# Performance work log

Measured on AMD Instinct MI355X. Metric: run time of the kernel, lower is better.

The kernel has to match this reference:

```python
import jax, jax.numpy as jnp
import numpy as np

ITERATIONS = 3  # init_kwargs: adjacency power order

def setup_inputs() -> dict:
    key = jax.random.key(0)
    ks = jax.random.split(key, 8)
    n_nodes = 100000
    in_ch, out_ch = 512, 128
    nnz_feat = 1600000
    n_edges = 1600000
    feat_rows = jax.random.randint(ks[0], (nnz_feat,), 0, n_nodes, dtype=jnp.int32)
    feat_cols = jax.random.randint(ks[1], (nnz_feat,), 0, in_ch, dtype=jnp.int32)
    feat_values = jax.random.uniform(ks[2], (nnz_feat,), dtype=jnp.float32)
    adj_rows = jax.random.randint(ks[3], (n_edges,), 0, n_nodes, dtype=jnp.int32)
    adj_cols = jax.random.randint(ks[4], (n_edges,), 0, n_nodes, dtype=jnp.int32)
    # normalized adjacency values (positive, roughly 1/degree scale)
    adj_values = jax.random.uniform(ks[5], (n_edges,), dtype=jnp.float32) / 16.0
    # xavier-uniform-like init
    bound_w = float(np.sqrt(6.0 / (in_ch + out_ch)))
    weight = jax.random.uniform(ks[6], (in_ch, out_ch), minval=-bound_w, maxval=bound_w, dtype=jnp.float32)
    bound_b = float(np.sqrt(6.0 / (1 + out_ch)))
    bias = jax.random.uniform(ks[7], (1, out_ch), minval=-bound_b, maxval=bound_b, dtype=jnp.float32)
    return {"feat_rows": feat_rows, "feat_cols": feat_cols, "feat_values": feat_values,
            "adj_rows": adj_rows, "adj_cols": adj_cols, "adj_values": adj_values,
            "weight": weight, "bias": bias, "n_nodes": n_nodes}

def reference(feat_rows, feat_cols, feat_values, adj_rows, adj_cols, adj_values, weight, bias, n_nodes):
    # SpMM: (sparse features [n_nodes, in_ch]) @ weight [in_ch, out_ch]
    # base[r] = sum over nnz with row r of val * weight[col]
    contrib = feat_values[:, None] * weight[feat_cols]           # [nnz, out_ch]
    base = jax.ops.segment_sum(contrib, feat_rows, num_segments=n_nodes)  # [n_nodes, out_ch]
    # bias + dropout (eval mode: identity) + relu
    base = jax.nn.relu(base + bias)
    # iterative sparse propagation: base = A_norm @ base, (iterations - 1) times
    for _ in range(ITERATIONS - 1):
        msgs = adj_values[:, None] * base[adj_cols]              # [n_edges, out_ch]
        base = jax.ops.segment_sum(msgs, adj_rows, num_segments=n_nodes)
    return base
```

## Files before the change

kernel.cpp:

```cpp
#include <hip/hip_runtime.h>
#include <hip/hip_fp16.h>


#define CH 128
#define BR 128
#define SCAN_BLK 1024
#define BIN_WGS 256
#define BIN_THR 512


__global__ void hist2_kernel(const int* __restrict__ rows_f, int nf, int chunk_f,
                             const int* __restrict__ rows_a, int na, int chunk_a,
                             int* __restrict__ wgc, int nbuck) {
    extern __shared__ int hcnt[];
    const int m  = blockIdx.x >> 8;
    const int wg = blockIdx.x & (BIN_WGS - 1);
    const int* rows = m ? rows_a : rows_f;
    const int nE    = m ? na : nf;
    const int chunk = m ? chunk_a : chunk_f;
    const int tid = threadIdx.x;
    const long long T = blockDim.x;
    long long start = (long long)wg * chunk;
    long long end = start + chunk;
    if (end > nE) end = nE;
    for (int b = tid; b < nbuck; b += blockDim.x) hcnt[b] = 0;
    __syncthreads();
    if (start < end) {
        long long i = start + tid;
        for (; i + 3 * T < end; i += 4 * T) {
            int r0 = rows[i], r1 = rows[i + T], r2 = rows[i + 2 * T], r3 = rows[i + 3 * T];
            atomicAdd(&hcnt[r0 >> 7], 1);
            atomicAdd(&hcnt[r1 >> 7], 1);
            atomicAdd(&hcnt[r2 >> 7], 1);
            atomicAdd(&hcnt[r3 >> 7], 1);
        }
        for (; i < end; i += T) atomicAdd(&hcnt[rows[i] >> 7], 1);
    }
    __syncthreads();
    int* out = wgc + ((long long)m * BIN_WGS + wg) * nbuck;
    for (int b = tid; b < nbuck; b += blockDim.x) out[b] = hcnt[b];
}

__global__ void wgscan2_kernel(int* __restrict__ wgc, int* __restrict__ bcounts,
                               int nbuck, int nwg) {
    int wpb = blockDim.x >> 6;
    int idx = blockIdx.x * wpb + (threadIdx.x >> 6);
    int lane = threadIdx.x & 63;
    if (idx >= 2 * nbuck) return;
    int m = (idx >= nbuck) ? 1 : 0;
    int b = idx - m * nbuck;
    int* base = wgc + (long long)m * nwg * nbuck + b;
    int carry = 0;
    for (int w0 = 0; w0 < nwg; w0 += 64) {
        int wg = w0 + lane;
        int v = (wg < nwg) ? base[(long long)wg * nbuck] : 0;
        int x = v;
        #pragma unroll
        for (int off = 1; off < 64; off <<= 1) {
            int y = __shfl_up(x, off);
            if (lane >= off) x += y;
        }
        if (wg < nwg) base[(long long)wg * nbuck] = carry + x - v;
        carry += __shfl(x, 63);
    }
    if (lane == 0) bcounts[idx] = carry;
}

__global__ void bucket_scan2_kernel(const int* __restrict__ bcounts,
                                    int* __restrict__ bbase, int nbuck) {
    __shared__ int lds[SCAN_BLK];
    int m = blockIdx.x;
    int tid = threadIdx.x;
    int x = (tid < nbuck) ? bcounts[m * nbuck + tid] : 0;
    lds[tid] = x;
    __syncthreads();
    for (int off = 1; off < SCAN_BLK; off <<= 1) {
        int y = (tid >= off) ? lds[tid - off] : 0;
        __syncthreads();
        lds[tid] += y;
        __syncthreads();
    }
    int* bb = bbase + m * (nbuck + 1);
    if (tid < nbuck) bb[tid] = lds[tid] - x;
    if (tid == nbuck - 1) bb[nbuck] = lds[tid];
}

__global__ void bin2_kernel(const int* __restrict__ rows_f, const int* __restrict__ cols_f,
                            const float* __restrict__ vals_f, int nf, int chunk_f,
                            const int* __restrict__ rows_a, const int* __restrict__ cols_a,
                            const float* __restrict__ vals_a, int na, int chunk_a,
                            const int* __restrict__ bbase, const int* __restrict__ wgc,
                            int2* __restrict__ cvt_f, int2* __restrict__ cvt_a, int nbuck) {
    extern __shared__ int lds[];
    int* hcnt  = lds;
    int* hbase = lds + nbuck;
    const int m  = blockIdx.x >> 8;
    const int wg = blockIdx.x & (BIN_WGS - 1);
    const int* rows = m ? rows_a : rows_f;
    const int* cols = m ? cols_a : cols_f;
    const float* vals = m ? vals_a : vals_f;
    const int nE    = m ? na : nf;
    const int chunk = m ? chunk_a : chunk_f;
    int2* cv_tmp = m ? cvt_a : cvt_f;
    const int* bb = bbase + m * (nbuck + 1);
    const int* wc = wgc + ((long long)m * BIN_WGS + wg) * nbuck;
    const int tid = threadIdx.x;
    const long long T = blockDim.x;
    long long start = (long long)wg * chunk;
    long long end = start + chunk;
    if (end > nE) end = nE;
    for (int b = tid; b < nbuck; b += blockDim.x) {
        hbase[b] = bb[b] + wc[b];
        hcnt[b] = 0;
    }
    __syncthreads();
    if (start >= end) return;
    long long i = start + tid;
    for (; i + 3 * T < end; i += 4 * T) {
        int r0 = rows[i], r1 = rows[i + T], r2 = rows[i + 2 * T], r3 = rows[i + 3 * T];
        int c0 = cols[i], c1 = cols[i + T], c2 = cols[i + 2 * T], c3 = cols[i + 3 * T];
        float v0 = vals[i], v1 = vals[i + T], v2 = vals[i + 2 * T], v3 = vals[i + 3 * T];
        int b0 = r0 >> 7, b1 = r1 >> 7, b2 = r2 >> 7, b3 = r3 >> 7;
        int p0 = hbase[b0] + atomicAdd(&hcnt[b0], 1);
        int p1 = hbase[b1] + atomicAdd(&hcnt[b1], 1);
        int p2 = hbase[b2] + atomicAdd(&hcnt[b2], 1);
        int p3 = hbase[b3] + atomicAdd(&hcnt[b3], 1);
        cv_tmp[p0] = make_int2(c0 | ((r0 & (BR - 1)) << 24), __float_as_int(v0));
        cv_tmp[p1] = make_int2(c1 | ((r1 & (BR - 1)) << 24), __float_as_int(v1));
        cv_tmp[p2] = make_int2(c2 | ((r2 & (BR - 1)) << 24), __float_as_int(v2));
        cv_tmp[p3] = make_int2(c3 | ((r3 & (BR - 1)) << 24), __float_as_int(v3));
    }
    for (; i < end; i += T) {
        int r = rows[i];
        int b = r >> 7;
        int p = hbase[b] + atomicAdd(&hcnt[b], 1);
        cv_tmp[p] = make_int2(cols[i] | ((r & (BR - 1)) << 24), __float_as_int(vals[i]));
    }
}

__global__ void reorder2_kernel(const int* __restrict__ bucket_base,
                                const int2* __restrict__ cv_tmp, int2* __restrict__ cv,
                                int* __restrict__ row_ptr, int n) {
    __shared__ int cnt[BR];
    __shared__ int tmp[BR];
    int b = blockIdx.x;
    int rbase = b * BR;
    int tid = threadIdx.x;
    int s = bucket_base[b], e = bucket_base[b + 1];
    if (tid < BR) cnt[tid] = 0;
    __syncthreads();
    for (int i = s + tid; i < e; i += blockDim.x)
        atomicAdd(&cnt[((unsigned)cv_tmp[i].x) >> 24], 1);
    __syncthreads();
    if (tid < BR) tmp[tid] = cnt[tid];
    __syncthreads();
    for (int off = 1; off < BR; off <<= 1) {
        int y = 0;
        if (tid < BR && tid >= off) y = tmp[tid - off];
        __syncthreads();
        if (tid < BR) tmp[tid] += y;
        __syncthreads();
    }
    if (tid < BR) {
        int excl = s + tmp[tid] - cnt[tid];
        if (rbase + tid < n) row_ptr[rbase + tid] = excl;
        cnt[tid] = excl;
    }
    if (tid == 0 && b == gridDim.x - 1) row_ptr[n] = e;
    __syncthreads();
    for (int i = s + tid; i < e; i += blockDim.x) {
        int2 ent = cv_tmp[i];
        int rl = ((unsigned)ent.x) >> 24;
        int p = atomicAdd(&cnt[rl], 1);
        cv[p] = make_int2(ent.x & 0x00FFFFFF, ent.y);
    }
}


__global__ void wconv_kernel(const float* __restrict__ W, __half2* __restrict__ Wh, int n2) {
    int i = blockIdx.x * blockDim.x + threadIdx.x;
    if (i < n2) Wh[i] = __float22half2_rn(reinterpret_cast<const float2*>(W)[i]);
}


#define GATHER_BODY(TBL)                                                            \
    for (int base = s; base < e; base += 64) {                                      \
        int idx = base + lane;                                                      \
        mysc[lane] = (idx < e) ? cv[idx] : 0;                                       \
        int m = e - base; if (m > 64) m = 64;                                       \
        int nb = (m + 15) >> 4;                                                     \
        for (int t = 0; t < nb; t++) {                                              \
            int k0 = t << 4;                                                        \
            long long ck0 = mysc[k0 + g];                                           \
            long long ck1 = mysc[k0 + 4 + g];                                       \
            long long ck2 = mysc[k0 + 8 + g];                                       \
            long long ck3 = mysc[k0 + 12 + g];                                      \
            float4 sv0 = *reinterpret_cast<const float4*>(TBL + (long long)(int)ck0 * 64 + cl * 4); \
            float4 sv1 = *reinterpret_cast<const float4*>(TBL + (long long)(int)ck1 * 64 + cl * 4); \
            float4 sv2 = *reinterpret_cast<const float4*>(TBL + (long long)(int)ck2 * 64 + cl * 4); \
            float4 sv3 = *reinterpret_cast<const float4*>(TBL + (long long)(int)ck3 * 64 + cl * 4); \
            float v0 = __int_as_float((int)(ck0 >> 32));                            \
            float v1 = __int_as_float((int)(ck1 >> 32));                            \
            float v2 = __int_as_float((int)(ck2 >> 32));                            \
            float v3 = __int_as_float((int)(ck3 >> 32));                            \
            ACC8(v0, sv0); ACC8(v1, sv1); ACC8(v2, sv2); ACC8(v3, sv3);             \
        }                                                                           \
    }

#define ACC8(V, SV) {                                                               \
    float2 f0 = __half22float2(*reinterpret_cast<const __half2*>(&(SV).x));         \
    float2 f1 = __half22float2(*reinterpret_cast<const __half2*>(&(SV).y));         \
    float2 f2 = __half22float2(*reinterpret_cast<const __half2*>(&(SV).z));         \
    float2 f3 = __half22float2(*reinterpret_cast<const __half2*>(&(SV).w));         \
    acc0 += (V) * f0.x; acc1 += (V) * f0.y;                                         \
    acc2 += (V) * f1.x; acc3 += (V) * f1.y;                                         \
    acc4 += (V) * f2.x; acc5 += (V) * f2.y;                                         \
    acc6 += (V) * f3.x; acc7 += (V) * f3.y; }

#define XREDUCE()                                                                   \
    acc0 += __shfl_xor(acc0, 16); acc1 += __shfl_xor(acc1, 16);                     \
    acc2 += __shfl_xor(acc2, 16); acc3 += __shfl_xor(acc3, 16);                     \
    acc4 += __shfl_xor(acc4, 16); acc5 += __shfl_xor(acc5, 16);                     \
    acc6 += __shfl_xor(acc6, 16); acc7 += __shfl_xor(acc7, 16);                     \
    acc0 += __shfl_xor(acc0, 32); acc1 += __shfl_xor(acc1, 32);                     \
    acc2 += __shfl_xor(acc2, 32); acc3 += __shfl_xor(acc3, 32);                     \
    acc4 += __shfl_xor(acc4, 32); acc5 += __shfl_xor(acc5, 32);                     \
    acc6 += __shfl_xor(acc6, 32); acc7 += __shfl_xor(acc7, 32);

__global__ void spmm_g4_kernel(const int* __restrict__ row_ptr,
                               const long long* __restrict__ cv,
                               const __half2* __restrict__ Wh,
                               const float* __restrict__ bias,
                               __half2* __restrict__ outh, int n) {
    __shared__ long long sc[4 * 64];
    int gtid = blockIdx.x * blockDim.x + threadIdx.x;
    int wid = gtid >> 6;
    int lane = gtid & 63;
    if (wid >= n) return;
    int g = lane >> 4;
    int cl = lane & 15;
    long long* mysc = sc + (threadIdx.x >> 6) * 64;
    int s = row_ptr[wid], e = row_ptr[wid + 1];
    float acc0 = 0.f, acc1 = 0.f, acc2 = 0.f, acc3 = 0.f;
    float acc4 = 0.f, acc5 = 0.f, acc6 = 0.f, acc7 = 0.f;
    GATHER_BODY(Wh)
    XREDUCE()
    if (g == 0) {
        const float4* bp = reinterpret_cast<const float4*>(bias);
        float4 b0 = bp[cl * 2], b1 = bp[cl * 2 + 1];
        acc0 = fmaxf(acc0 + b0.x, 0.f); acc1 = fmaxf(acc1 + b0.y, 0.f);
        acc2 = fmaxf(acc2 + b0.z, 0.f); acc3 = fmaxf(acc3 + b0.w, 0.f);
        acc4 = fmaxf(acc4 + b1.x, 0.f); acc5 = fmaxf(acc5 + b1.y, 0.f);
        acc6 = fmaxf(acc6 + b1.z, 0.f); acc7 = fmaxf(acc7 + b1.w, 0.f);
        __half2 h0 = __floats2half2_rn(acc0, acc1);
        __half2 h1 = __floats2half2_rn(acc2, acc3);
        __half2 h2 = __floats2half2_rn(acc4, acc5);
        __half2 h3 = __floats2half2_rn(acc6, acc7);
        float4 ov;
        *reinterpret_cast<__half2*>(&ov.x) = h0;
        *reinterpret_cast<__half2*>(&ov.y) = h1;
        *reinterpret_cast<__half2*>(&ov.z) = h2;
        *reinterpret_cast<__half2*>(&ov.w) = h3;
        *reinterpret_cast<float4*>(outh + (long long)wid * 64 + cl * 4) = ov;
    }
}

__global__ void prop_g4_h2h_kernel(const int* __restrict__ row_ptr,
                                   const long long* __restrict__ cv,
                                   const __half2* __restrict__ src, __half2* __restrict__ dst,
                                   int n) {
    __shared__ long long sc[4 * 64];
    int gtid = blockIdx.x * blockDim.x + threadIdx.x;
    int wid = gtid >> 6;
    int lane = gtid & 63;
    if (wid >= n) return;
    int g = lane >> 4;
    int cl = lane & 15;
    long long* mysc = sc + (threadIdx.x >> 6) * 64;
    int s = row_ptr[wid], e = row_ptr[wid + 1];
    float acc0 = 0.f, acc1 = 0.f, acc2 = 0.f, acc3 = 0.f;
    float acc4 = 0.f, acc5 = 0.f, acc6 = 0.f, acc7 = 0.f;
    GATHER_BODY(src)
    XREDUCE()
    if (g == 0) {
        __half2 h0 = __floats2half2_rn(acc0, acc1);
        __half2 h1 = __floats2half2_rn(acc2, acc3);
        __half2 h2 = __floats2half2_rn(acc4, acc5);
        __half2 h3 = __floats2half2_rn(acc6, acc7);
        float4 ov;
        *reinterpret_cast<__half2*>(&ov.x) = h0;
        *reinterpret_cast<__half2*>(&ov.y) = h1;
        *reinterpret_cast<__half2*>(&ov.z) = h2;
        *reinterpret_cast<__half2*>(&ov.w) = h3;
        *reinterpret_cast<float4*>(dst + (long long)wid * 64 + cl * 4) = ov;
    }
}

__global__ void prop_g4_h2f_kernel(const int* __restrict__ row_ptr,
                                   const long long* __restrict__ cv,
                                   const __half2* __restrict__ src, float* __restrict__ dst,
                                   int n) {
    __shared__ long long sc[4 * 64];
    int gtid = blockIdx.x * blockDim.x + threadIdx.x;
    int wid = gtid >> 6;
    int lane = gtid & 63;
    if (wid >= n) return;
    int g = lane >> 4;
    int cl = lane & 15;
    long long* mysc = sc + (threadIdx.x >> 6) * 64;
    int s = row_ptr[wid], e = row_ptr[wid + 1];
    float acc0 = 0.f, acc1 = 0.f, acc2 = 0.f, acc3 = 0.f;
    float acc4 = 0.f, acc5 = 0.f, acc6 = 0.f, acc7 = 0.f;
    GATHER_BODY(src)
    XREDUCE()
    if (g == 0) {
        float4 o0 = make_float4(acc0, acc1, acc2, acc3);
        float4 o1 = make_float4(acc4, acc5, acc6, acc7);
        float4* dp = reinterpret_cast<float4*>(dst + (long long)wid * 128 + cl * 8);
        dp[0] = o0;
        dp[1] = o1;
    }
}


__global__ void bias_relu_kernel(float* __restrict__ buf, const float* __restrict__ bias,
                                 long long total) {
    long long i = ((long long)blockIdx.x * blockDim.x + threadIdx.x) * 4;
    if (i >= total) return;
    float4 v = *reinterpret_cast<float4*>(buf + i);
    int ch = (int)(i & (CH - 1));
    float4 b = *reinterpret_cast<const float4*>(bias + ch);
    v.x = fmaxf(v.x + b.x, 0.0f);
    v.y = fmaxf(v.y + b.y, 0.0f);
    v.z = fmaxf(v.z + b.z, 0.0f);
    v.w = fmaxf(v.w + b.w, 0.0f);
    *reinterpret_cast<float4*>(buf + i) = v;
}

__global__ void spmm_scatter_kernel(const int* __restrict__ rows, const int* __restrict__ cols,
                                    const float* __restrict__ vals, const float* __restrict__ weight,
                                    float* __restrict__ out, int nnz) {
    long long tid = (long long)blockIdx.x * blockDim.x + threadIdx.x;
    if (tid >= (long long)nnz * 32) return;
    int e = (int)(tid >> 5), lane = (int)(tid & 31);
    int r = rows[e], c = cols[e];
    float v = vals[e];
    const float4 w = *reinterpret_cast<const float4*>(weight + (long long)c * CH + lane * 4);
    float* dst = out + (long long)r * CH + lane * 4;
    unsafeAtomicAdd(dst + 0, v * w.x);
    unsafeAtomicAdd(dst + 1, v * w.y);
    unsafeAtomicAdd(dst + 2, v * w.z);
    unsafeAtomicAdd(dst + 3, v * w.w);
}

__global__ void prop_scatter_kernel(const int* __restrict__ rows, const int* __restrict__ cols,
                                    const float* __restrict__ vals, const float* __restrict__ src,
                                    float* __restrict__ dst, int ne) {
    long long tid = (long long)blockIdx.x * blockDim.x + threadIdx.x;
    if (tid >= (long long)ne * 32) return;
    int e = (int)(tid >> 5), lane = (int)(tid & 31);
    int r = rows[e], c = cols[e];
    float v = vals[e];
    const float4 s = *reinterpret_cast<const float4*>(src + (long long)c * CH + lane * 4);
    float* d = dst + (long long)r * CH + lane * 4;
    unsafeAtomicAdd(d + 0, v * s.x);
    unsafeAtomicAdd(d + 1, v * s.y);
    unsafeAtomicAdd(d + 2, v * s.z);
    unsafeAtomicAdd(d + 3, v * s.w);
}


static inline size_t align64(size_t x) { return (x + 63) & ~(size_t)63; }

extern "C" void kernel_launch(void* const* d_in, const int* in_sizes, int n_in,
                              void* d_out, int out_size, void* d_ws, size_t ws_size,
                              hipStream_t stream) {
    const int*   feat_rows = (const int*)d_in[0];
    const int*   feat_cols = (const int*)d_in[1];
    const float* feat_vals = (const float*)d_in[2];
    const int*   adj_rows  = (const int*)d_in[3];
    const int*   adj_cols  = (const int*)d_in[4];
    const float* adj_vals  = (const float*)d_in[5];
    const float* weight    = (const float*)d_in[6];
    const float* bias      = (const float*)d_in[7];

    const int nnz = in_sizes[0];
    const int ne  = in_sizes[3];
    const int n   = out_size / CH;
    const int in_ch = in_sizes[6] / CH;

    float* out = (float*)d_out;
    char*  ws  = (char*)d_ws;

    const size_t NBF = (size_t)n * CH * sizeof(float);
    const size_t NBH = (size_t)n * CH * sizeof(__half);
    const long long total_elems = (long long)n * CH;
    const int BLK = 256;
    const int ew_blocks = (int)((total_elems / 4 + BLK - 1) / BLK);
    const int maxe = nnz > ne ? nnz : ne;
    const int nbuck = (n + BR - 1) / BR;
    const size_t bin_lds = (size_t)nbuck * 2 * sizeof(int);

    size_t off = 0;
    __half2* baseh   = (__half2*)(ws + off); off += align64(NBH);
    __half2* pingh   = (__half2*)(ws + off); off += align64(NBH);
    int*   row_ptr  = (int*)(ws + off);   off += align64(((size_t)n + 1) * 4);
    int*   bcounts  = (int*)(ws + off);   off += align64((size_t)2 * nbuck * 4);
    int*   bbase    = (int*)(ws + off);   off += align64((size_t)2 * (nbuck + 1) * 4);
    int*   wgc      = (int*)(ws + off);   off += align64((size_t)2 * BIN_WGS * nbuck * 4);
    __half2* Wh     = (__half2*)(ws + off); off += align64((size_t)in_ch * 64 * 4);
    int2*  cv       = (int2*)(ws + off);  off += align64((size_t)maxe * 8);
    int2*  cvt_f    = (int2*)pingh;
    int2*  cvt_a    = (int2*)((char*)pingh + (size_t)nnz * 8);
    const bool fast = (ws_size >= off) && (nbuck <= SCAN_BLK) &&
                      (n <= (1 << 24)) && (bin_lds <= 64 * 1024) &&
                      (in_ch <= (1 << 22)) &&
                      (((size_t)nnz + (size_t)ne) * 8 <= NBH);

    if (fast) {
        const int row_blocks = (int)(((long long)n * 64 + BLK - 1) / BLK);
        const int chunk_feat = (nnz + BIN_WGS - 1) / BIN_WGS;
        const int chunk_adj  = (ne + BIN_WGS - 1) / BIN_WGS;
        const int w2 = in_ch * 64;
        const size_t hist_lds = (size_t)nbuck * sizeof(int);
        const int wgscan_blocks = (2 * nbuck + 3) / 4;

        wconv_kernel<<<(w2 + BLK - 1) / BLK, BLK, 0, stream>>>(weight, Wh, w2);

        hist2_kernel<<<2 * BIN_WGS, BIN_THR, hist_lds, stream>>>(
            feat_rows, nnz, chunk_feat, adj_rows, ne, chunk_adj, wgc, nbuck);
        wgscan2_kernel<<<wgscan_blocks, 256, 0, stream>>>(wgc, bcounts, nbuck, BIN_WGS);
        bucket_scan2_kernel<<<2, SCAN_BLK, 0, stream>>>(bcounts, bbase, nbuck);
        bin2_kernel<<<2 * BIN_WGS, BIN_THR, bin_lds, stream>>>(
            feat_rows, feat_cols, feat_vals, nnz, chunk_feat,
            adj_rows, adj_cols, adj_vals, ne, chunk_adj,
            bbase, wgc, cvt_f, cvt_a, nbuck);

        reorder2_kernel<<<nbuck, BIN_THR, 0, stream>>>(bbase, cvt_f, cv, row_ptr, n);
        spmm_g4_kernel<<<row_blocks, BLK, 0, stream>>>(
            row_ptr, (const long long*)cv, Wh, bias, baseh, n);

        reorder2_kernel<<<nbuck, BIN_THR, 0, stream>>>(bbase + (nbuck + 1), cvt_a, cv, row_ptr, n);
        prop_g4_h2h_kernel<<<row_blocks, BLK, 0, stream>>>(
            row_ptr, (const long long*)cv, baseh, pingh, n);
        prop_g4_h2f_kernel<<<row_blocks, BLK, 0, stream>>>(
            row_ptr, (const long long*)cv, pingh, out, n);
    } else {
        float* ping = (float*)ws;
        const int spmm_blocks = (int)(((long long)nnz * 32 + BLK - 1) / BLK);
        const int prop_blocks = (int)(((long long)ne * 32 + BLK - 1) / BLK);
        hipMemsetAsync(d_out, 0, NBF, stream);
        spmm_scatter_kernel<<<spmm_blocks, BLK, 0, stream>>>(feat_rows, feat_cols, feat_vals,
                                                             weight, out, nnz);
        bias_relu_kernel<<<ew_blocks, BLK, 0, stream>>>(out, bias, total_elems);
        hipMemsetAsync(ping, 0, NBF, stream);
        prop_scatter_kernel<<<prop_blocks, BLK, 0, stream>>>(adj_rows, adj_cols, adj_vals,
                                                             out, ping, ne);
        hipMemsetAsync(d_out, 0, NBF, stream);
        prop_scatter_kernel<<<prop_blocks, BLK, 0, stream>>>(adj_rows, adj_cols, adj_vals,
                                                             ping, out, ne);
    }
}
```

Before: 237.0 us.

## Process four CSR rows per wavefront instead of one row split four ways

Measured after the change: 232.3 us. 2.0% less time.

```diff
diff --git a/kernel.cpp b/kernel.cpp
--- a/kernel.cpp
+++ b/kernel.cpp
@@ -183,18 +183,29 @@
 }
 
 
-#define GATHER_BODY(TBL)                                                            \
-    for (int base = s; base < e; base += 64) {                                      \
+#define ACC8(V, SV) {                                                               \
+    float2 f0 = __half22float2(*reinterpret_cast<const __half2*>(&(SV).x));         \
+    float2 f1 = __half22float2(*reinterpret_cast<const __half2*>(&(SV).y));         \
+    float2 f2 = __half22float2(*reinterpret_cast<const __half2*>(&(SV).z));         \
+    float2 f3 = __half22float2(*reinterpret_cast<const __half2*>(&(SV).w));         \
+    acc0 += (V) * f0.x; acc1 += (V) * f0.y;                                         \
+    acc2 += (V) * f1.x; acc3 += (V) * f1.y;                                         \
+    acc4 += (V) * f2.x; acc5 += (V) * f2.y;                                         \
+    acc6 += (V) * f3.x; acc7 += (V) * f3.y; }
+
+#define R4_BODY(TBL)                                                                \
+    for (int base = s4; base < e4; base += 64) {                                    \
         int idx = base + lane;                                                      \
-        mysc[lane] = (idx < e) ? cv[idx] : 0;                                       \
-        int m = e - base; if (m > 64) m = 64;                                       \
-        int nb = (m + 15) >> 4;                                                     \
-        for (int t = 0; t < nb; t++) {                                              \
-            int k0 = t << 4;                                                        \
-            long long ck0 = mysc[k0 + g];                                           \
-            long long ck1 = mysc[k0 + 4 + g];                                       \
-            long long ck2 = mysc[k0 + 8 + g];                                       \
-            long long ck3 = mysc[k0 + 12 + g];                                      \
+        mysc[lane] = (idx < e4) ? cv[idx] : 0;                                      \
+        int klo = rs > base ? rs : base;                                            \
+        int lim = base + 64;                                                        \
+        int khi = re < lim ? re : lim;                                              \
+        int k = klo;                                                                \
+        for (; k + 4 <= khi; k += 4) {                                              \
+            long long ck0 = mysc[k - base + 0];                                     \
+            long long ck1 = mysc[k - base + 1];                                     \
+            long long ck2 = mysc[k - base + 2];                                     \
+            long long ck3 = mysc[k - base + 3];                                     \
             float4 sv0 = *reinterpret_cast<const float4*>(TBL + (long long)(int)ck0 * 64 + cl * 4); \
             float4 sv1 = *reinterpret_cast<const float4*>(TBL + (long long)(int)ck1 * 64 + cl * 4); \
             float4 sv2 = *reinterpret_cast<const float4*>(TBL + (long long)(int)ck2 * 64 + cl * 4); \
@@ -205,47 +216,43 @@
             float v3 = __int_as_float((int)(ck3 >> 32));                            \
             ACC8(v0, sv0); ACC8(v1, sv1); ACC8(v2, sv2); ACC8(v3, sv3);             \
         }                                                                           \
-    }
-
-#define ACC8(V, SV) {                                                               \
-    float2 f0 = __half22float2(*reinterpret_cast<const __half2*>(&(SV).x));         \
-    float2 f1 = __half22float2(*reinterpret_cast<const __half2*>(&(SV).y));         \
-    float2 f2 = __half22float2(*reinterpret_cast<const __half2*>(&(SV).z));         \
-    float2 f3 = __half22float2(*reinterpret_cast<const __half2*>(&(SV).w));         \
-    acc0 += (V) * f0.x; acc1 += (V) * f0.y;                                         \
-    acc2 += (V) * f1.x; acc3 += (V) * f1.y;                                         \
-    acc4 += (V) * f2.x; acc5 += (V) * f2.y;                                         \
-    acc6 += (V) * f3.x; acc7 += (V) * f3.y; }
-
-#define XREDUCE()                                                                   \
-    acc0 += __shfl_xor(acc0, 16); acc1 += __shfl_xor(acc1, 16);                     \
-    acc2 += __shfl_xor(acc2, 16); acc3 += __shfl_xor(acc3, 16);                     \
-    acc4 += __shfl_xor(acc4, 16); acc5 += __shfl_xor(acc5, 16);                     \
-    acc6 += __shfl_xor(acc6, 16); acc7 += __shfl_xor(acc7, 16);                     \
-    acc0 += __shfl_xor(acc0, 32); acc1 += __shfl_xor(acc1, 32);                     \
-    acc2 += __shfl_xor(acc2, 32); acc3 += __shfl_xor(acc3, 32);                     \
-    acc4 += __shfl_xor(acc4, 32); acc5 += __shfl_xor(acc5, 32);                     \
-    acc6 += __shfl_xor(acc6, 32); acc7 += __shfl_xor(acc7, 32);
-
-__global__ void spmm_g4_kernel(const int* __restrict__ row_ptr,
+        for (; k < khi; k++) {                                                      \
+            long long ck = mysc[k - base];                                          \
+            float v = __int_as_float((int)(ck >> 32));                              \
+            float4 sv = *reinterpret_cast<const float4*>(TBL + (long long)(int)ck * 64 + cl * 4); \
+            ACC8(v, sv);                                                            \
+        }                                                                           \
+    }
+
+#define R4_PROLOGUE()                                                               \
+    int gtid = blockIdx.x * blockDim.x + threadIdx.x;                               \
+    int wid0 = (gtid >> 6) << 2;                                                    \
+    int lane = gtid & 63;                                                           \
+    if (wid0 >= n) return;                                                          \
+    int g = lane >> 4;                                                              \
+    int cl = lane & 15;                                                             \
+    long long* mysc = sc + ((threadIdx.x >> 6) << 6);                               \
+    int r = wid0 + g;                                                               \
+    bool valid = (r < n);                                                           \
+    int rv = valid ? r : (n - 1);                                                   \
+    int rs = row_ptr[rv];                                                           \
+    int re = row_ptr[rv + 1];                                                       \
+    if (!valid) { rs = 0; re = 0; }                                                 \
+    int s4 = row_ptr[wid0];                                                         \
+    int rend = wid0 + 4 < n ? wid0 + 4 : n;                                         \
+    int e4 = row_ptr[rend];                                                         \
+    float acc0 = 0.f, acc1 = 0.f, acc2 = 0.f, acc3 = 0.f;                           \
+    float acc4 = 0.f, acc5 = 0.f, acc6 = 0.f, acc7 = 0.f;
+
+__global__ void spmm_r4_kernel(const int* __restrict__ row_ptr,
                                const long long* __restrict__ cv,
                                const __half2* __restrict__ Wh,
                                const float* __restrict__ bias,
                                __half2* __restrict__ outh, int n) {
     __shared__ long long sc[4 * 64];
-    int gtid = blockIdx.x * blockDim.x + threadIdx.x;
-    int wid = gtid >> 6;
-    int lane = gtid & 63;
-    if (wid >= n) return;
-    int g = lane >> 4;
-    int cl = lane & 15;
-    long long* mysc = sc + (threadIdx.x >> 6) * 64;
-    int s = row_ptr[wid], e = row_ptr[wid + 1];
-    float acc0 = 0.f, acc1 = 0.f, acc2 = 0.f, acc3 = 0.f;
-    float acc4 = 0.f, acc5 = 0.f, acc6 = 0.f, acc7 = 0.f;
-    GATHER_BODY(Wh)
-    XREDUCE()
-    if (g == 0) {
+    R4_PROLOGUE()
+    R4_BODY(Wh)
+    if (valid) {
         const float4* bp = reinterpret_cast<const float4*>(bias);
         float4 b0 = bp[cl * 2], b1 = bp[cl * 2 + 1];
         acc0 = fmaxf(acc0 + b0.x, 0.f); acc1 = fmaxf(acc1 + b0.y, 0.f);
@@ -261,28 +268,18 @@
         *reinterpret_cast<__half2*>(&ov.y) = h1;
         *reinterpret_cast<__half2*>(&ov.z) = h2;
         *reinterpret_cast<__half2*>(&ov.w) = h3;
-        *reinterpret_cast<float4*>(outh + (long long)wid * 64 + cl * 4) = ov;
-    }
-}
-
-__global__ void prop_g4_h2h_kernel(const int* __restrict__ row_ptr,
+        *reinterpret_cast<float4*>(outh + (long long)r * 64 + cl * 4) = ov;
+    }
+}
+
+__global__ void prop_r4_h2h_kernel(const int* __restrict__ row_ptr,
                                    const long long* __restrict__ cv,
                                    const __half2* __restrict__ src, __half2* __restrict__ dst,
                                    int n) {
     __shared__ long long sc[4 * 64];
-    int gtid = blockIdx.x * blockDim.x + threadIdx.x;
-    int wid = gtid >> 6;
-    int lane = gtid & 63;
-    if (wid >= n) return;
-    int g = lane >> 4;
-    int cl = lane & 15;
-    long long* mysc = sc + (threadIdx.x >> 6) * 64;
-    int s = row_ptr[wid], e = row_ptr[wid + 1];
-    float acc0 = 0.f, acc1 = 0.f, acc2 = 0.f, acc3 = 0.f;
-    float acc4 = 0.f, acc5 = 0.f, acc6 = 0.f, acc7 = 0.f;
-    GATHER_BODY(src)
-    XREDUCE()
-    if (g == 0) {
+    R4_PROLOGUE()
+    R4_BODY(src)
+    if (valid) {
         __half2 h0 = __floats2half2_rn(acc0, acc1);
         __half2 h1 = __floats2half2_rn(acc2, acc3);
         __half2 h2 = __floats2half2_rn(acc4, acc5);
@@ -292,31 +289,21 @@
         *reinterpret_cast<__half2*>(&ov.y) = h1;
         *reinterpret_cast<__half2*>(&ov.z) = h2;
         *reinterpret_cast<__half2*>(&ov.w) = h3;
-        *reinterpret_cast<float4*>(dst + (long long)wid * 64 + cl * 4) = ov;
-    }
-}
-
-__global__ void prop_g4_h2f_kernel(const int* __restrict__ row_ptr,
+        *reinterpret_cast<float4*>(dst + (long long)r * 64 + cl * 4) = ov;
+    }
+}
+
+__global__ void prop_r4_h2f_kernel(const int* __restrict__ row_ptr,
                                    const long long* __restrict__ cv,
                                    const __half2* __restrict__ src, float* __restrict__ dst,
                                    int n) {
     __shared__ long long sc[4 * 64];
-    int gtid = blockIdx.x * blockDim.x + threadIdx.x;
-    int wid = gtid >> 6;
-    int lane = gtid & 63;
-    if (wid >= n) return;
-    int g = lane >> 4;
-    int cl = lane & 15;
-    long long* mysc = sc + (threadIdx.x >> 6) * 64;
-    int s = row_ptr[wid], e = row_ptr[wid + 1];
-    float acc0 = 0.f, acc1 = 0.f, acc2 = 0.f, acc3 = 0.f;
-    float acc4 = 0.f, acc5 = 0.f, acc6 = 0.f, acc7 = 0.f;
-    GATHER_BODY(src)
-    XREDUCE()
-    if (g == 0) {
+    R4_PROLOGUE()
+    R4_BODY(src)
+    if (valid) {
         float4 o0 = make_float4(acc0, acc1, acc2, acc3);
         float4 o1 = make_float4(acc4, acc5, acc6, acc7);
-        float4* dp = reinterpret_cast<float4*>(dst + (long long)wid * 128 + cl * 8);
+        float4* dp = reinterpret_cast<float4*>(dst + (long long)r * 128 + cl * 8);
         dp[0] = o0;
         dp[1] = o1;
     }
@@ -418,7 +405,8 @@
                       (((size_t)nnz + (size_t)ne) * 8 <= NBH);
 
     if (fast) {
-        const int row_blocks = (int)(((long long)n * 64 + BLK - 1) / BLK);
+        const int nwaves = (n + 3) / 4;
+        const int row_blocks = (int)(((long long)nwaves * 64 + BLK - 1) / BLK);
         const int chunk_feat = (nnz + BIN_WGS - 1) / BIN_WGS;
         const int chunk_adj  = (ne + BIN_WGS - 1) / BIN_WGS;
         const int w2 = in_ch * 64;
@@ -437,13 +425,13 @@
             bbase, wgc, cvt_f, cvt_a, nbuck);
 
         reorder2_kernel<<<nbuck, BIN_THR, 0, stream>>>(bbase, cvt_f, cv, row_ptr, n);
-        spmm_g4_kernel<<<row_blocks, BLK, 0, stream>>>(
+        spmm_r4_kernel<<<row_blocks, BLK, 0, stream>>>(
             row_ptr, (const long long*)cv, Wh, bias, baseh, n);
 
         reorder2_kernel<<<nbuck, BIN_THR, 0, stream>>>(bbase + (nbuck + 1), cvt_a, cv, row_ptr, n);
-        prop_g4_h2h_kernel<<<row_blocks, BLK, 0, stream>>>(
+        prop_r4_h2h_kernel<<<row_blocks, BLK, 0, stream>>>(
             row_ptr, (const long long*)cv, baseh, pingh, n);
-        prop_g4_h2f_kernel<<<row_blocks, BLK, 0, stream>>>(
+        prop_r4_h2f_kernel<<<row_blocks, BLK, 0, stream>>>(
             row_ptr, (const long long*)cv, pingh, out, n);
     } else {
         float* ping = (float*)ws;
```
